# Kernel optimization log

Hardware: AMD Instinct MI355X
Metric: run time of the kernel (lower is better)

The kernel has to match this reference:

```python
import jax, jax.numpy as jnp
import numpy as np

FX, FY, CX, CY = 320.0, 320.0, 320.0, 240.0
N_MP, N_KF, M = 200000, 2000, 4000000


def setup_inputs() -> dict:
    key = jax.random.key(0)
    k1, k2, k3, k4 = jax.random.split(key, 4)
    # Map-point positions; shift to [1,2) so the homogeneous z after the (near-identity)
    # pose transform stays well away from zero for a stable perspective divide.
    tMP = jax.random.uniform(k1, (N_MP, 3), dtype=jnp.float32) + 1.0
    # Keyframe poses: identity + small perturbation (realistic SE3-like 4x4 matrices).
    tKF = jnp.eye(4, dtype=jnp.float32)[None] + 0.05 * jax.random.normal(k2, (N_KF, 4, 4), dtype=jnp.float32)
    # Measurement edges: (kf_id, mp_id) pairs.
    kf_ids = jax.random.randint(k3, (M,), 0, N_KF, dtype=jnp.int32)
    mp_ids = jax.random.randint(k4, (M,), 0, N_MP, dtype=jnp.int32)
    # Unique, sorted id columns (MPs[:,0] / KFs[:,0] in the original module).
    idxKF = jnp.arange(N_KF, dtype=jnp.int32)
    idxMP = jnp.arange(N_MP, dtype=jnp.int32)
    return {"tMP": tMP, "tKF": tKF, "kf_ids": kf_ids, "mp_ids": mp_ids,
            "idxKF": idxKF, "idxMP": idxMP}


def reference(tMP, tKF, kf_ids, mp_ids, idxKF, idxMP):
    # ID match. Original builds an O(M*N) boolean equality tensor and takes
    # torch.where(...)[1]; for unique sorted id arrays this is exactly a
    # sorted-index lookup, so we use searchsorted (same result, no huge temp).
    indexKF = jnp.searchsorted(idxKF, kf_ids)   # [M]
    indexMP = jnp.searchsorted(idxMP, mp_ids)   # [M]
    # Homogeneous map points: pad with 1 (F.pad(..., value=1) in original).
    tMPhomo = jnp.concatenate([tMP, jnp.ones((tMP.shape[0], 1), tMP.dtype)], axis=1)  # [N_MP,4]
    # Gather per-edge pose / point and do batched 4x4 @ 4 matvec.
    P = jnp.einsum('mij,mj->mi', tKF[indexKF], tMPhomo[indexMP])  # [M,4]
    # Perspective divide + intrinsics.
    ptx = P[:, 0] / P[:, 2] * FX + CX
    pty = P[:, 1] / P[:, 2] * FY + CY
    return jnp.stack([ptx, pty], axis=1)  # [M,2]
```

## Files before the change

### kernel.cpp

```cpp
#include <hip/hip_runtime.h>


#define FX_ 320.0f
#define FY_ 320.0f
#define CX_ 320.0f
#define CY_ 240.0f

#define MAX_KF 2000
#define MAIN_BLOCK 1024
#define PERSIST_GRID 256
#define EPT 8

__global__ __launch_bounds__(256) void mp_pack_kernel(
    const float* __restrict__ tMP, float4* __restrict__ tMPh, int N)
{
    int i = blockIdx.x * blockDim.x + threadIdx.x;
    if (i < N) {
        const float* p = tMP + (size_t)i * 3;
        tMPh[i] = make_float4(p[0], p[1], p[2], 1.0f);
    }
}

__device__ __forceinline__ void project2(
    const float4* sKF, int kf, const float4& p, float* rx, float* ry)
{
    float4 r0 = sKF[kf * 3 + 0];
    float4 r1 = sKF[kf * 3 + 1];
    float4 r2 = sKF[kf * 3 + 2];
    float P0 = fmaf(r0.x, p.x, fmaf(r0.y, p.y, fmaf(r0.z, p.z, r0.w)));
    float P1 = fmaf(r1.x, p.x, fmaf(r1.y, p.y, fmaf(r1.z, p.z, r1.w)));
    float P2 = fmaf(r2.x, p.x, fmaf(r2.y, p.y, fmaf(r2.z, p.z, r2.w)));
    float inv = 1.0f / P2;
    *rx = fmaf(P0 * inv, FX_, CX_);
    *ry = fmaf(P1 * inv, FY_, CY_);
}

__global__ __launch_bounds__(MAIN_BLOCK, 4) void ba_project_persist_kernel(
    const float4* __restrict__ tMPh,
    const float*  __restrict__ tKF,
    const int*    __restrict__ kf_ids,
    const int*    __restrict__ mp_ids,
    float* __restrict__ out,
    int M, int N_KF)
{
    __shared__ float4 sKF[MAX_KF * 3];

    int nChunks = N_KF * 3;
    for (int i = threadIdx.x; i < nChunks; i += MAIN_BLOCK) {
        int k = i / 3;
        int r = i - k * 3;
        sKF[i] = *reinterpret_cast<const float4*>(tKF + (size_t)k * 16 + r * 4);
    }
    __syncthreads();

    size_t tid = (size_t)blockIdx.x * MAIN_BLOCK + threadIdx.x;
    size_t stride = (size_t)PERSIST_GRID * MAIN_BLOCK * EPT;

    for (size_t m0 = tid * EPT; m0 < (size_t)M; m0 += stride) {
        if (m0 + EPT <= (size_t)M) {
            int4 kfa = *reinterpret_cast<const int4*>(kf_ids + m0);
            int4 kfb = *reinterpret_cast<const int4*>(kf_ids + m0 + 4);
            int4 mpa = *reinterpret_cast<const int4*>(mp_ids + m0);
            int4 mpb = *reinterpret_cast<const int4*>(mp_ids + m0 + 4);
            int kf[EPT] = {kfa.x, kfa.y, kfa.z, kfa.w, kfb.x, kfb.y, kfb.z, kfb.w};
            int mp[EPT] = {mpa.x, mpa.y, mpa.z, mpa.w, mpb.x, mpb.y, mpb.z, mpb.w};
            float4 p[EPT];
            #pragma unroll
            for (int i = 0; i < EPT; ++i) p[i] = tMPh[mp[i]];
            float4* o = reinterpret_cast<float4*>(out + m0 * 2);
            #pragma unroll
            for (int i = 0; i < EPT; i += 2) {
                float x0, y0, x1, y1;
                project2(sKF, kf[i + 0], p[i + 0], &x0, &y0);
                project2(sKF, kf[i + 1], p[i + 1], &x1, &y1);
                o[i >> 1] = make_float4(x0, y0, x1, y1);
            }
        } else {
            for (size_t m = m0; m < (size_t)M; ++m) {
                float4 p = tMPh[mp_ids[m]];
                float rx, ry;
                project2(sKF, kf_ids[m], p, &rx, &ry);
                out[m * 2 + 0] = rx;
                out[m * 2 + 1] = ry;
            }
        }
    }
}

__global__ __launch_bounds__(256) void ba_project_direct_kernel(
    const float* __restrict__ tMP, const float* __restrict__ tKF,
    const int* __restrict__ kf_ids, const int* __restrict__ mp_ids,
    float* __restrict__ out, int M)
{
    int t = blockIdx.x * blockDim.x + threadIdx.x;
    int m0 = t * 4;
    int mEnd = (m0 + 4 < M) ? (m0 + 4) : M;
    for (int m = m0; m < mEnd; ++m) {
        int kf = kf_ids[m];
        int mp = mp_ids[m];
        const float* K = tKF + (size_t)kf * 16;
        float4 r0 = *reinterpret_cast<const float4*>(K + 0);
        float4 r1 = *reinterpret_cast<const float4*>(K + 4);
        float4 r2 = *reinterpret_cast<const float4*>(K + 8);
        const float* p = tMP + (size_t)mp * 3;
        float x = p[0], y = p[1], z = p[2];
        float P0 = fmaf(r0.x, x, fmaf(r0.y, y, fmaf(r0.z, z, r0.w)));
        float P1 = fmaf(r1.x, x, fmaf(r1.y, y, fmaf(r1.z, z, r1.w)));
        float P2 = fmaf(r2.x, x, fmaf(r2.y, y, fmaf(r2.z, z, r2.w)));
        float inv = 1.0f / P2;
        out[2 * (size_t)m + 0] = fmaf(P0 * inv, FX_, CX_);
        out[2 * (size_t)m + 1] = fmaf(P1 * inv, FY_, CY_);
    }
}

extern "C" void kernel_launch(void* const* d_in, const int* in_sizes, int n_in,
                              void* d_out, int out_size, void* d_ws, size_t ws_size,
                              hipStream_t stream) {
    const float* tMP    = (const float*)d_in[0];
    const float* tKF    = (const float*)d_in[1];
    const int*   kf_ids = (const int*)d_in[2];
    const int*   mp_ids = (const int*)d_in[3];
    float* out = (float*)d_out;
    int M    = in_sizes[2];
    int N_MP = in_sizes[0] / 3;
    int N_KF = in_sizes[1] / 16;

    size_t need_ws = (size_t)N_MP * sizeof(float4);
    if (N_KF <= MAX_KF && ws_size >= need_ws) {
        float4* tMPh = (float4*)d_ws;
        mp_pack_kernel<<<(N_MP + 255) / 256, 256, 0, stream>>>(tMP, tMPh, N_MP);
        ba_project_persist_kernel<<<PERSIST_GRID, MAIN_BLOCK, 0, stream>>>(
            tMPh, tKF, kf_ids, mp_ids, out, M, N_KF);
    } else {
        int threads = (M + 3) / 4;
        int grid = (threads + 255) / 256;
        ba_project_direct_kernel<<<grid, 256, 0, stream>>>(
            tMP, tKF, kf_ids, mp_ids, out, M);
    }
}
```

Before: 121.5 us.

## Software-pipeline gather loads with nontemporal streaming and fast reciprocal

```diff
diff --git a/kernel.cpp b/kernel.cpp
--- a/kernel.cpp
+++ b/kernel.cpp
@@ -11,6 +11,9 @@
 #define PERSIST_GRID 256
 #define EPT 8
 
+typedef int   vint4   __attribute__((ext_vector_type(4)));
+typedef float vfloat4 __attribute__((ext_vector_type(4)));
+
 __global__ __launch_bounds__(256) void mp_pack_kernel(
     const float* __restrict__ tMP, float4* __restrict__ tMPh, int N)
 {
@@ -21,21 +24,59 @@
     }
 }
 
-__device__ __forceinline__ void project2(
-    const float4* sKF, int kf, const float4& p, float* rx, float* ry)
+struct Batch {
+    int kf[EPT];
+    float4 p[EPT];
+};
+
+__device__ __forceinline__ void issue_batch(
+    const int* __restrict__ kf_ids, const int* __restrict__ mp_ids,
+    const float4* __restrict__ tMPh, size_t m0, Batch& b)
 {
-    float4 r0 = sKF[kf * 3 + 0];
-    float4 r1 = sKF[kf * 3 + 1];
-    float4 r2 = sKF[kf * 3 + 2];
-    float P0 = fmaf(r0.x, p.x, fmaf(r0.y, p.y, fmaf(r0.z, p.z, r0.w)));
-    float P1 = fmaf(r1.x, p.x, fmaf(r1.y, p.y, fmaf(r1.z, p.z, r1.w)));
-    float P2 = fmaf(r2.x, p.x, fmaf(r2.y, p.y, fmaf(r2.z, p.z, r2.w)));
-    float inv = 1.0f / P2;
-    *rx = fmaf(P0 * inv, FX_, CX_);
-    *ry = fmaf(P1 * inv, FY_, CY_);
+    vint4 ka = __builtin_nontemporal_load(reinterpret_cast<const vint4*>(kf_ids + m0));
+    vint4 kb = __builtin_nontemporal_load(reinterpret_cast<const vint4*>(kf_ids + m0 + 4));
+    vint4 ma = __builtin_nontemporal_load(reinterpret_cast<const vint4*>(mp_ids + m0));
+    vint4 mb = __builtin_nontemporal_load(reinterpret_cast<const vint4*>(mp_ids + m0 + 4));
+    b.kf[0] = ka.x; b.kf[1] = ka.y; b.kf[2] = ka.z; b.kf[3] = ka.w;
+    b.kf[4] = kb.x; b.kf[5] = kb.y; b.kf[6] = kb.z; b.kf[7] = kb.w;
+    int mp[EPT] = {ma.x, ma.y, ma.z, ma.w, mb.x, mb.y, mb.z, mb.w};
+    #pragma unroll
+    for (int i = 0; i < EPT; ++i) b.p[i] = tMPh[mp[i]];
 }
 
-__global__ __launch_bounds__(MAIN_BLOCK, 4) void ba_project_persist_kernel(
+__device__ __forceinline__ void compute_store(
+    const float4* __restrict__ sKF, const Batch& b,
+    float* __restrict__ out, size_t m0)
+{
+    vfloat4 o[EPT / 2];
+    #pragma unroll
+    for (int i = 0; i < EPT; i += 2) {
+        float r[4];
+        #pragma unroll
+        for (int h = 0; h < 2; ++h) {
+            int kf = b.kf[i + h];
+            float4 pv = b.p[i + h];
+            float4 r0 = sKF[kf * 3 + 0];
+            float4 r1 = sKF[kf * 3 + 1];
+            float4 r2 = sKF[kf * 3 + 2];
+            float P0 = fmaf(r0.x, pv.x, fmaf(r0.y, pv.y, fmaf(r0.z, pv.z, r0.w)));
+            float P1 = fmaf(r1.x, pv.x, fmaf(r1.y, pv.y, fmaf(r1.z, pv.z, r1.w)));
+            float P2 = fmaf(r2.x, pv.x, fmaf(r2.y, pv.y, fmaf(r2.z, pv.z, r2.w)));
+            float inv = __builtin_amdgcn_rcpf(P2);
+            r[2 * h + 0] = fmaf(P0 * inv, FX_, CX_);
+            r[2 * h + 1] = fmaf(P1 * inv, FY_, CY_);
+        }
+        vfloat4 v;
+        v.x = r[0]; v.y = r[1]; v.z = r[2]; v.w = r[3];
+        o[i >> 1] = v;
+    }
+    vfloat4* op = reinterpret_cast<vfloat4*>(out + m0 * 2);
+    #pragma unroll
+    for (int j = 0; j < EPT / 2; ++j)
+        __builtin_nontemporal_store(o[j], op + j);
+}
+
+__global__ __launch_bounds__(MAIN_BLOCK, 4) void ba_project_pipe_kernel(
     const float4* __restrict__ tMPh,
     const float*  __restrict__ tKF,
     const int*    __restrict__ kf_ids,
@@ -53,36 +94,39 @@
     }
     __syncthreads();
 
+    const size_t nThreads = (size_t)PERSIST_GRID * MAIN_BLOCK;
+    const size_t stride = nThreads * EPT;
     size_t tid = (size_t)blockIdx.x * MAIN_BLOCK + threadIdx.x;
-    size_t stride = (size_t)PERSIST_GRID * MAIN_BLOCK * EPT;
+    size_t m0 = tid * EPT;
 
-    for (size_t m0 = tid * EPT; m0 < (size_t)M; m0 += stride) {
-        if (m0 + EPT <= (size_t)M) {
-            int4 kfa = *reinterpret_cast<const int4*>(kf_ids + m0);
-            int4 kfb = *reinterpret_cast<const int4*>(kf_ids + m0 + 4);
-            int4 mpa = *reinterpret_cast<const int4*>(mp_ids + m0);
-            int4 mpb = *reinterpret_cast<const int4*>(mp_ids + m0 + 4);
-            int kf[EPT] = {kfa.x, kfa.y, kfa.z, kfa.w, kfb.x, kfb.y, kfb.z, kfb.w};
-            int mp[EPT] = {mpa.x, mpa.y, mpa.z, mpa.w, mpb.x, mpb.y, mpb.z, mpb.w};
-            float4 p[EPT];
-            #pragma unroll
-            for (int i = 0; i < EPT; ++i) p[i] = tMPh[mp[i]];
-            float4* o = reinterpret_cast<float4*>(out + m0 * 2);
-            #pragma unroll
-            for (int i = 0; i < EPT; i += 2) {
-                float x0, y0, x1, y1;
-                project2(sKF, kf[i + 0], p[i + 0], &x0, &y0);
-                project2(sKF, kf[i + 1], p[i + 1], &x1, &y1);
-                o[i >> 1] = make_float4(x0, y0, x1, y1);
-            }
-        } else {
-            for (size_t m = m0; m < (size_t)M; ++m) {
-                float4 p = tMPh[mp_ids[m]];
-                float rx, ry;
-                project2(sKF, kf_ids[m], p, &rx, &ry);
-                out[m * 2 + 0] = rx;
-                out[m * 2 + 1] = ry;
-            }
+    if (m0 + EPT <= (size_t)M) {
+        Batch cur;
+        issue_batch(kf_ids, mp_ids, tMPh, m0, cur);
+        size_t m1 = m0 + stride;
+        while (m1 + EPT <= (size_t)M) {
+            Batch nxt;
+            issue_batch(kf_ids, mp_ids, tMPh, m1, nxt);
+            compute_store(sKF, cur, out, m0);
+            cur = nxt;
+            m0 = m1;
+            m1 += stride;
+        }
+        compute_store(sKF, cur, out, m0);
+    }
+
+    if (tid == 0) {
+        for (size_t m = (size_t)(M / EPT) * EPT; m < (size_t)M; ++m) {
+            int kf = kf_ids[m];
+            float4 pv = tMPh[mp_ids[m]];
+            float4 r0 = sKF[kf * 3 + 0];
+            float4 r1 = sKF[kf * 3 + 1];
+            float4 r2 = sKF[kf * 3 + 2];
+            float P0 = fmaf(r0.x, pv.x, fmaf(r0.y, pv.y, fmaf(r0.z, pv.z, r0.w)));
+            float P1 = fmaf(r1.x, pv.x, fmaf(r1.y, pv.y, fmaf(r1.z, pv.z, r1.w)));
+            float P2 = fmaf(r2.x, pv.x, fmaf(r2.y, pv.y, fmaf(r2.z, pv.z, r2.w)));
+            float inv = __builtin_amdgcn_rcpf(P2);
+            out[m * 2 + 0] = fmaf(P0 * inv, FX_, CX_);
+            out[m * 2 + 1] = fmaf(P1 * inv, FY_, CY_);
         }
     }
 }
@@ -129,7 +173,7 @@
     if (N_KF <= MAX_KF && ws_size >= need_ws) {
         float4* tMPh = (float4*)d_ws;
         mp_pack_kernel<<<(N_MP + 255) / 256, 256, 0, stream>>>(tMP, tMPh, N_MP);
-        ba_project_persist_kernel<<<PERSIST_GRID, MAIN_BLOCK, 0, stream>>>(
+        ba_project_pipe_kernel<<<PERSIST_GRID, MAIN_BLOCK, 0, stream>>>(
             tMPh, tKF, kf_ids, mp_ids, out, M, N_KF);
     } else {
         int threads = (M + 3) / 4;
```

Result: slower. 131.3 us (+8.1%).

## Pack pose rows in fp16 to shrink LDS and launch a non-persistent grid

Applied to the files above, without the earlier changes.

```diff
diff --git a/kernel.cpp b/kernel.cpp
--- a/kernel.cpp
+++ b/kernel.cpp
@@ -8,8 +8,33 @@
 
 #define MAX_KF 2000
 #define MAIN_BLOCK 1024
-#define PERSIST_GRID 256
 #define EPT 8
+
+typedef int      vint4  __attribute__((ext_vector_type(4)));
+typedef _Float16 half8v __attribute__((ext_vector_type(8)));
+
+struct alignas(16) KFE {
+    half8v r01;
+    float4 r2;
+};
+
+__global__ __launch_bounds__(256) void kf_pack_kernel(
+    const float* __restrict__ tKF, KFE* __restrict__ kfe, int N_KF)
+{
+    int k = blockIdx.x * blockDim.x + threadIdx.x;
+    if (k >= N_KF) return;
+    const float* K = tKF + (size_t)k * 16;
+    float4 r0 = *reinterpret_cast<const float4*>(K + 0);
+    float4 r1 = *reinterpret_cast<const float4*>(K + 4);
+    float4 r2 = *reinterpret_cast<const float4*>(K + 8);
+    KFE e;
+    e.r01[0] = (_Float16)r0.x; e.r01[1] = (_Float16)r0.y;
+    e.r01[2] = (_Float16)r0.z; e.r01[3] = (_Float16)r0.w;
+    e.r01[4] = (_Float16)r1.x; e.r01[5] = (_Float16)r1.y;
+    e.r01[6] = (_Float16)r1.z; e.r01[7] = (_Float16)r1.w;
+    e.r2 = r2;
+    kfe[k] = e;
+}
 
 __global__ __launch_bounds__(256) void mp_pack_kernel(
     const float* __restrict__ tMP, float4* __restrict__ tMPh, int N)
@@ -21,68 +46,66 @@
     }
 }
 
-__device__ __forceinline__ void project2(
-    const float4* sKF, int kf, const float4& p, float* rx, float* ry)
+__device__ __forceinline__ void project1(
+    const KFE* __restrict__ sKF, int kf, const float4& pv, float* rx, float* ry)
 {
-    float4 r0 = sKF[kf * 3 + 0];
-    float4 r1 = sKF[kf * 3 + 1];
-    float4 r2 = sKF[kf * 3 + 2];
-    float P0 = fmaf(r0.x, p.x, fmaf(r0.y, p.y, fmaf(r0.z, p.z, r0.w)));
-    float P1 = fmaf(r1.x, p.x, fmaf(r1.y, p.y, fmaf(r1.z, p.z, r1.w)));
-    float P2 = fmaf(r2.x, p.x, fmaf(r2.y, p.y, fmaf(r2.z, p.z, r2.w)));
-    float inv = 1.0f / P2;
+    half8v h = sKF[kf].r01;
+    float4 r2 = sKF[kf].r2;
+    float P0 = fmaf((float)h[0], pv.x, fmaf((float)h[1], pv.y,
+                fmaf((float)h[2], pv.z, (float)h[3])));
+    float P1 = fmaf((float)h[4], pv.x, fmaf((float)h[5], pv.y,
+                fmaf((float)h[6], pv.z, (float)h[7])));
+    float P2 = fmaf(r2.x, pv.x, fmaf(r2.y, pv.y, fmaf(r2.z, pv.z, r2.w)));
+    float inv = __builtin_amdgcn_rcpf(P2);
     *rx = fmaf(P0 * inv, FX_, CX_);
     *ry = fmaf(P1 * inv, FY_, CY_);
 }
 
-__global__ __launch_bounds__(MAIN_BLOCK, 4) void ba_project_persist_kernel(
+__global__ __launch_bounds__(MAIN_BLOCK, 8) void ba_project_occ_kernel(
     const float4* __restrict__ tMPh,
-    const float*  __restrict__ tKF,
+    const KFE*    __restrict__ kfe,
     const int*    __restrict__ kf_ids,
     const int*    __restrict__ mp_ids,
     float* __restrict__ out,
     int M, int N_KF)
 {
-    __shared__ float4 sKF[MAX_KF * 3];
-
-    int nChunks = N_KF * 3;
-    for (int i = threadIdx.x; i < nChunks; i += MAIN_BLOCK) {
-        int k = i / 3;
-        int r = i - k * 3;
-        sKF[i] = *reinterpret_cast<const float4*>(tKF + (size_t)k * 16 + r * 4);
+    __shared__ KFE sKF[MAX_KF];
+    {
+        const float4* src = reinterpret_cast<const float4*>(kfe);
+        float4* dst = reinterpret_cast<float4*>(sKF);
+        int nc = N_KF * 2;
+        for (int i = threadIdx.x; i < nc; i += MAIN_BLOCK) dst[i] = src[i];
     }
     __syncthreads();
 
     size_t tid = (size_t)blockIdx.x * MAIN_BLOCK + threadIdx.x;
-    size_t stride = (size_t)PERSIST_GRID * MAIN_BLOCK * EPT;
+    size_t m0 = tid * EPT;
 
-    for (size_t m0 = tid * EPT; m0 < (size_t)M; m0 += stride) {
-        if (m0 + EPT <= (size_t)M) {
-            int4 kfa = *reinterpret_cast<const int4*>(kf_ids + m0);
-            int4 kfb = *reinterpret_cast<const int4*>(kf_ids + m0 + 4);
-            int4 mpa = *reinterpret_cast<const int4*>(mp_ids + m0);
-            int4 mpb = *reinterpret_cast<const int4*>(mp_ids + m0 + 4);
-            int kf[EPT] = {kfa.x, kfa.y, kfa.z, kfa.w, kfb.x, kfb.y, kfb.z, kfb.w};
-            int mp[EPT] = {mpa.x, mpa.y, mpa.z, mpa.w, mpb.x, mpb.y, mpb.z, mpb.w};
-            float4 p[EPT];
-            #pragma unroll
-            for (int i = 0; i < EPT; ++i) p[i] = tMPh[mp[i]];
-            float4* o = reinterpret_cast<float4*>(out + m0 * 2);
-            #pragma unroll
-            for (int i = 0; i < EPT; i += 2) {
-                float x0, y0, x1, y1;
-                project2(sKF, kf[i + 0], p[i + 0], &x0, &y0);
-                project2(sKF, kf[i + 1], p[i + 1], &x1, &y1);
-                o[i >> 1] = make_float4(x0, y0, x1, y1);
-            }
-        } else {
-            for (size_t m = m0; m < (size_t)M; ++m) {
-                float4 p = tMPh[mp_ids[m]];
-                float rx, ry;
-                project2(sKF, kf_ids[m], p, &rx, &ry);
-                out[m * 2 + 0] = rx;
-                out[m * 2 + 1] = ry;
-            }
+    if (m0 + EPT <= (size_t)M) {
+        vint4 ka = __builtin_nontemporal_load(reinterpret_cast<const vint4*>(kf_ids + m0));
+        vint4 kb = __builtin_nontemporal_load(reinterpret_cast<const vint4*>(kf_ids + m0 + 4));
+        vint4 ma = __builtin_nontemporal_load(reinterpret_cast<const vint4*>(mp_ids + m0));
+        vint4 mb = __builtin_nontemporal_load(reinterpret_cast<const vint4*>(mp_ids + m0 + 4));
+        int kf[EPT] = {ka.x, ka.y, ka.z, ka.w, kb.x, kb.y, kb.z, kb.w};
+        int mp[EPT] = {ma.x, ma.y, ma.z, ma.w, mb.x, mb.y, mb.z, mb.w};
+        float4 p[EPT];
+        #pragma unroll
+        for (int i = 0; i < EPT; ++i) p[i] = tMPh[mp[i]];
+        float res[2 * EPT];
+        #pragma unroll
+        for (int i = 0; i < EPT; ++i)
+            project1(sKF, kf[i], p[i], &res[2 * i], &res[2 * i + 1]);
+        float4* o = reinterpret_cast<float4*>(out + m0 * 2);
+        #pragma unroll
+        for (int j = 0; j < EPT / 2; ++j)
+            o[j] = make_float4(res[4 * j], res[4 * j + 1], res[4 * j + 2], res[4 * j + 3]);
+    } else if (m0 < (size_t)M) {
+        for (size_t m = m0; m < (size_t)M; ++m) {
+            float4 pv = tMPh[mp_ids[m]];
+            float rx, ry;
+            project1(sKF, kf_ids[m], pv, &rx, &ry);
+            out[m * 2 + 0] = rx;
+            out[m * 2 + 1] = ry;
         }
     }
 }
@@ -125,12 +148,19 @@
     int N_MP = in_sizes[0] / 3;
     int N_KF = in_sizes[1] / 16;
 
-    size_t need_ws = (size_t)N_MP * sizeof(float4);
+    const size_t KFE_BYTES = 65536;
+    size_t need_ws = KFE_BYTES + (size_t)N_MP * sizeof(float4);
+
     if (N_KF <= MAX_KF && ws_size >= need_ws) {
-        float4* tMPh = (float4*)d_ws;
+        KFE*    kfe  = (KFE*)d_ws;
+        float4* tMPh = (float4*)((char*)d_ws + KFE_BYTES);
+        kf_pack_kernel<<<(N_KF + 255) / 256, 256, 0, stream>>>(tKF, kfe, N_KF);
         mp_pack_kernel<<<(N_MP + 255) / 256, 256, 0, stream>>>(tMP, tMPh, N_MP);
-        ba_project_persist_kernel<<<PERSIST_GRID, MAIN_BLOCK, 0, stream>>>(
-            tMPh, tKF, kf_ids, mp_ids, out, M, N_KF);
+        int perBlock = MAIN_BLOCK * EPT;
+        int nb = (M + perBlock - 1) / perBlock;
+        nb = ((nb + 511) / 512) * 512;
+        ba_project_occ_kernel<<<nb, MAIN_BLOCK, 0, stream>>>(
+            tMPh, kfe, kf_ids, mp_ids, out, M, N_KF);
     } else {
         int threads = (M + 3) / 4;
         int grid = (threads + 255) / 256;
```

Measured after the change: 129.7 us. 1.07x slower.
